# Kernel optimization log

Hardware: AMD Instinct MI355X
Metric: run time of the kernel (lower is better)

The kernel has to match this reference:

```python
import jax, jax.numpy as jnp
import numpy as np

B, N, D, H, DH, DEPTH = 4, 1024, 1024, 16, 64, 4
FI = int(D * 4.0 * 2 / 3)  # 2730, GEGLU inner dim
EPS = 1.1920929e-07  # torch float32 eps (RMSNorm default)
NEG = -jnp.finfo(jnp.float32).max


def rms(x, w):
    return x * jax.lax.rsqrt(jnp.mean(x * x, axis=-1, keepdims=True) + EPS) * w


def rope(t):
    # t: [b, h, n, d]; interleaved-pair rotary (lucidrains rotary_embedding_torch)
    n, d = t.shape[-2], t.shape[-1]
    inv_freq = 1.0 / (10000.0 ** (jnp.arange(0, d, 2, dtype=jnp.float32) / d))
    ang = jnp.arange(n, dtype=jnp.float32)[:, None] * inv_freq  # [n, d/2]
    cos = jnp.repeat(jnp.cos(ang), 2, axis=-1)  # [n, d]
    sin = jnp.repeat(jnp.sin(ang), 2, axis=-1)
    x = t.reshape(t.shape[:-1] + (d // 2, 2))
    rot = jnp.stack([-x[..., 1], x[..., 0]], axis=-1).reshape(t.shape)
    return t * cos + rot * sin


def setup_inputs() -> dict:
    key = jax.random.key(0)
    ks = jax.random.split(key, 14)
    s = 0.02
    return {
        "x": jax.random.normal(ks[0], (B, N, D), dtype=jnp.float32),
        "norm_attn_w": jnp.ones((DEPTH, D), jnp.float32),
        "wq": jax.random.normal(ks[1], (DEPTH, H * DH, D), jnp.float32) * s,
        "wkv": jax.random.normal(ks[2], (DEPTH, 2 * H * DH, D), jnp.float32) * s,
        "wo": jax.random.normal(ks[3], (DEPTH, D, H * DH), jnp.float32) * s,
        "wg": jax.random.normal(ks[4], (DEPTH, H, D), jnp.float32) * s,
        "wmix": jax.random.normal(ks[5], (DEPTH, H, D), jnp.float32) * s,
        "norm_ff_w": jnp.ones((DEPTH, D), jnp.float32),
        "ff_norm_w": jnp.ones((DEPTH, D), jnp.float32),
        "w_in": jax.random.normal(ks[6], (DEPTH, 2 * FI, D), jnp.float32) * s,
        "b_in": jnp.zeros((DEPTH, 2 * FI), jnp.float32),
        "w_out": jax.random.normal(ks[7], (DEPTH, D, FI), jnp.float32) * s,
        "b_out": jnp.zeros((DEPTH, D), jnp.float32),
        "final_norm_w": jnp.ones((D,), jnp.float32),
    }


def _forward(x, norm_attn_w, wq, wkv, wo, wg, wmix, norm_ff_w, ff_norm_w,
             w_in, b_in, w_out, b_out, final_norm_w):
    scale = DH ** -0.5
    causal = jnp.triu(jnp.ones((N, N), bool), k=1)  # True = masked
    value_residual = None
    for i in range(DEPTH):
        # --- attention block (pre-RMSNorm wrapper) ---
        h = rms(x, norm_attn_w[i])  # [b, n, d]
        q = jnp.einsum('bnd,ed->bne', h, wq[i]) * scale
        kv = jnp.einsum('bnd,ed->bne', h, wkv[i])
        k, v = jnp.split(kv, 2, axis=-1)
        split = lambda t: t.reshape(B, N, H, DH).transpose(0, 2, 1, 3)  # b h n d
        q, k, v = split(q), split(k), split(v)
        orig_v = v
        if value_residual is not None:
            mix = jax.nn.sigmoid(jnp.einsum('bnd,hd->bhn', h, wmix[i]))[..., None]
            v = v + mix * (value_residual - v)  # lerp(v, value_residual, mix)
        q, k = rope(q), rope(k)
        sim = jnp.einsum('bhid,bhjd->bhij', q, k)
        sim = jnp.where(causal, NEG, sim)
        attn = jax.nn.softmax(sim, axis=-1)
        out = jnp.einsum('bhij,bhjd->bhid', attn, v)
        gates = jax.nn.sigmoid(jnp.einsum('bnd,hd->bhn', h, wg[i]))[..., None]
        out = out * gates
        out = out.transpose(0, 2, 1, 3).reshape(B, N, H * DH)
        x = x + jnp.einsum('bne,de->bnd', out, wo[i])
        if value_residual is None:
            value_residual = orig_v
        # --- feedforward block (wrapper norm + FF's own pre-rmsnorm) ---
        g = rms(x, norm_ff_w[i])
        g = rms(g, ff_norm_w[i])
        u = jnp.einsum('bnd,ed->bne', g, w_in[i]) + b_in[i]
        a, gt = jnp.split(u, 2, axis=-1)
        u = a * jax.nn.gelu(gt, approximate=False)
        x = x + jnp.einsum('bnf,df->bnd', u, w_out[i]) + b_out[i]
    return rms(x, final_norm_w)


def reference(x, norm_attn_w, wq, wkv, wo, wg, wmix, norm_ff_w, ff_norm_w,
              w_in, b_in, w_out, b_out, final_norm_w):
    return _forward(x, norm_attn_w, wq, wkv, wo, wg, wmix, norm_ff_w,
                    ff_norm_w, w_in, b_in, w_out, b_out, final_norm_w)
```

## Files before the change

kernel.cpp:

```cpp
#include <hip/hip_runtime.h>
#include <cstdint>
#include <cstddef>


#define DEV_INLINE __device__ __forceinline__

typedef short bf16x8 __attribute__((ext_vector_type(8)));
typedef float f32x4 __attribute__((ext_vector_type(4)));

constexpr int Bsz = 4, Nseq = 1024, Dm = 1024, Hh = 16, DH = 64, NDEPTH = 4;
constexpr int FI = 2730;
constexpr int FI_PAD = 2752;
constexpr int FI_TILE = 2816;
constexpr int WIDE = 2 * FI_TILE;
constexpr int ROWS = Bsz * Nseq;
constexpr float EPSR = 1.1920929e-07f;

DEV_INLINE float bf2f(unsigned short u) {
  unsigned int x = ((unsigned int)u) << 16;
  float f; __builtin_memcpy(&f, &x, 4); return f;
}
DEV_INLINE unsigned short f2bf(float f) {
  unsigned int x; __builtin_memcpy(&x, &f, 4);
  unsigned int r = x + 0x7fffu + ((x >> 16) & 1u);
  return (unsigned short)(r >> 16);
}

using gptr_t = const __attribute__((address_space(1))) void*;
using lptr_t = __attribute__((address_space(3))) void*;
DEV_INLINE void gl_lds16(const void* g, void* l) {
  __builtin_amdgcn_global_load_lds((gptr_t)g, (lptr_t)l, 16, 0, 0);
}
DEV_INLINE void fence_mem() { asm volatile("" ::: "memory"); }

__global__ __launch_bounds__(256)
void convf2b(const float* __restrict__ src, unsigned short* __restrict__ dst,
             int src_rows, int src_cols, int dst_cols) {
  const int r = blockIdx.y;
  const int c8 = (blockIdx.x * blockDim.x + threadIdx.x) * 8;
  if (c8 >= dst_cols) return;
  alignas(16) unsigned short o[8];
  if (r < src_rows && c8 + 8 <= src_cols) {
    const float2* p = (const float2*)&src[(size_t)r * src_cols + c8];
    const float2 v0 = p[0], v1 = p[1], v2 = p[2], v3 = p[3];
    o[0] = f2bf(v0.x); o[1] = f2bf(v0.y); o[2] = f2bf(v1.x); o[3] = f2bf(v1.y);
    o[4] = f2bf(v2.x); o[5] = f2bf(v2.y); o[6] = f2bf(v3.x); o[7] = f2bf(v3.y);
  } else {
#pragma unroll
    for (int j = 0; j < 8; ++j) {
      const int c = c8 + j;
      float v = (r < src_rows && c < src_cols) ? src[(size_t)r * src_cols + c] : 0.0f;
      o[j] = f2bf(v);
    }
  }
  *(uint4*)&dst[(size_t)r * dst_cols + c8] = *(const uint4*)o;
}

__global__ __launch_bounds__(128)
void convf2b_g16(const float* __restrict__ src, unsigned short* __restrict__ dst) {
  const int p = blockIdx.y;
  const int c8 = threadIdx.x * 8;
  const int t = p >> 5, r5 = p & 31;
  const int half = (r5 < 16) ? 1 : 0;
  const int srow = t * 16 + (r5 & 15);
  alignas(16) unsigned short o[8];
  if (srow < FI) {
    const size_t base = ((size_t)((r5 < 16) ? 0 : 1) * FI + srow) * 1024 + c8;
    const float4 v0 = *(const float4*)&src[base];
    const float4 v1 = *(const float4*)&src[base + 4];
    o[0]=f2bf(v0.x); o[1]=f2bf(v0.y); o[2]=f2bf(v0.z); o[3]=f2bf(v0.w);
    o[4]=f2bf(v1.x); o[5]=f2bf(v1.y); o[6]=f2bf(v1.z); o[7]=f2bf(v1.w);
  } else {
#pragma unroll
    for (int j = 0; j < 8; ++j) o[j] = 0;
  }
  (void)half;
  *(uint4*)&dst[(size_t)p * 1024 + c8] = *(const uint4*)o;
}

__global__ __launch_bounds__(256)
void rope_tables(float* __restrict__ cost, float* __restrict__ sint) {
  int idx = blockIdx.x * 256 + threadIdx.x;
  if (idx >= Nseq * 32) return;
  int n = idx >> 5, p = idx & 31;
  float freq = powf(10000.0f, -(float)(2 * p) * (1.0f / 64.0f));
  float ang = (float)n * freq;
  cost[idx] = cosf(ang);
  sint[idx] = sinf(ang);
}

__global__ __launch_bounds__(256)
void rms_one(const float* __restrict__ x, const float* __restrict__ w,
             unsigned short* __restrict__ out) {
  __shared__ float sred[4];
  const int row = blockIdx.x, tid = threadIdx.x;
  const float4 v = ((const float4*)(x + (size_t)row * Dm))[tid];
  float ss = v.x * v.x + v.y * v.y + v.z * v.z + v.w * v.w;
#pragma unroll
  for (int o = 32; o >= 1; o >>= 1) ss += __shfl_xor(ss, o, 64);
  if ((tid & 63) == 0) sred[tid >> 6] = ss;
  __syncthreads();
  float rs = rsqrtf((sred[0] + sred[1] + sred[2] + sred[3]) * (1.0f / Dm) + EPSR);
  const float4 wv = ((const float4*)w)[tid];
  alignas(8) unsigned short o4[4] = { f2bf(v.x * rs * wv.x), f2bf(v.y * rs * wv.y),
                                      f2bf(v.z * rs * wv.z), f2bf(v.w * rs * wv.w) };
  *(uint2*)&out[(size_t)row * Dm + tid * 4] = *(const uint2*)o4;
}

__global__ __launch_bounds__(256)
void rms_ff(const float* __restrict__ x, const float* __restrict__ w1,
            const float* __restrict__ w2, unsigned short* __restrict__ out) {
  __shared__ float sred[4];
  const int row = blockIdx.x, tid = threadIdx.x;
  const float4 v = ((const float4*)(x + (size_t)row * Dm))[tid];
  const float4 w1v = ((const float4*)w1)[tid];
  const float4 w2v = ((const float4*)w2)[tid];
  float ss = v.x * v.x + v.y * v.y + v.z * v.z + v.w * v.w;
#pragma unroll
  for (int o = 32; o >= 1; o >>= 1) ss += __shfl_xor(ss, o, 64);
  if ((tid & 63) == 0) sred[tid >> 6] = ss;
  __syncthreads();
  float rs1 = rsqrtf((sred[0] + sred[1] + sred[2] + sred[3]) * (1.0f / Dm) + EPSR);
  float t0 = v.x * rs1 * w1v.x, t1 = v.y * rs1 * w1v.y;
  float t2 = v.z * rs1 * w1v.z, t3 = v.w * rs1 * w1v.w;
  float ss2 = t0 * t0 + t1 * t1 + t2 * t2 + t3 * t3;
#pragma unroll
  for (int o = 32; o >= 1; o >>= 1) ss2 += __shfl_xor(ss2, o, 64);
  __syncthreads();
  if ((tid & 63) == 0) sred[tid >> 6] = ss2;
  __syncthreads();
  float rs2 = rsqrtf((sred[0] + sred[1] + sred[2] + sred[3]) * (1.0f / Dm) + EPSR);
  alignas(8) unsigned short o4[4] = { f2bf(t0 * rs2 * w2v.x), f2bf(t1 * rs2 * w2v.y),
                                      f2bf(t2 * rs2 * w2v.z), f2bf(t3 * rs2 * w2v.w) };
  *(uint2*)&out[(size_t)row * Dm + tid * 4] = *(const uint2*)o4;
}

__global__ __launch_bounds__(256)
void rms_final(const float* __restrict__ x, const float* __restrict__ w,
               float* __restrict__ out) {
  __shared__ float sred[4];
  const int row = blockIdx.x, tid = threadIdx.x;
  const float4 v = ((const float4*)(x + (size_t)row * Dm))[tid];
  float ss = v.x * v.x + v.y * v.y + v.z * v.z + v.w * v.w;
#pragma unroll
  for (int o = 32; o >= 1; o >>= 1) ss += __shfl_xor(ss, o, 64);
  if ((tid & 63) == 0) sred[tid >> 6] = ss;
  __syncthreads();
  float rs = rsqrtf((sred[0] + sred[1] + sred[2] + sred[3]) * (1.0f / Dm) + EPSR);
  const float4 wv = ((const float4*)w)[tid];
  float4 o;
  o.x = v.x * rs * wv.x; o.y = v.y * rs * wv.y;
  o.z = v.z * rs * wv.z; o.w = v.w * rs * wv.w;
  ((float4*)(out + (size_t)row * Dm))[tid] = o;
}

template <int MODE>
__global__ __launch_bounds__(256)
void gemm_nt(const unsigned short* __restrict__ A,
             const unsigned short* __restrict__ Bw,
             void* __restrict__ Cout,
             const float* __restrict__ bias,
             const float* __restrict__ resid,
             int K, int ldc, int n_store) {
  __shared__ unsigned short As[2][128 * 64];
  __shared__ unsigned short Bs[2][128 * 64];
  const int tid = threadIdx.x;
  const int m0 = blockIdx.x * 128;
  const int n0 = blockIdx.y * 128;
  const int w = tid >> 6, l = tid & 63;
  const int wm = (w >> 1) * 64, wn = (w & 1) * 64;
  const int lr = l & 15, lg = l >> 4;
  const int lsub = l & 7, lrow8 = l >> 3;
  const int colsw = (lsub ^ lrow8) << 3;
  const unsigned short* gA = &A[(size_t)(m0 + w * 8 + lrow8) * K + colsw];
  const unsigned short* gB = &Bw[(size_t)(n0 + w * 8 + lrow8) * K + colsw];
  const size_t rstep = (size_t)32 * K;
  f32x4 acc[4][4] = {};

  auto stage = [&](int buf, int kt) {
    const int o = kt * 64;
#pragma unroll
    for (int i = 0; i < 4; ++i) {
      gl_lds16(gA + i * rstep + o, &As[buf][i * 2048 + w * 512]);
      gl_lds16(gB + i * rstep + o, &Bs[buf][i * 2048 + w * 512]);
    }
  };
  auto compute = [&](int buf) {
    bf16x8 af[2][4], bfr[2][4];
#pragma unroll
    for (int ks = 0; ks < 2; ++ks) {
      const int slot = (ks * 4 + lg) ^ (lr & 7);
#pragma unroll
      for (int fj = 0; fj < 4; ++fj)
        bfr[ks][fj] = *(const bf16x8*)&Bs[buf][(wn + fj * 16 + lr) * 64 + slot * 8];
#pragma unroll
      for (int fi = 0; fi < 4; ++fi)
        af[ks][fi] = *(const bf16x8*)&As[buf][(wm + fi * 16 + lr) * 64 + slot * 8];
    }
    __builtin_amdgcn_s_setprio(1);
#pragma unroll
    for (int ks = 0; ks < 2; ++ks)
#pragma unroll
      for (int fi = 0; fi < 4; ++fi)
#pragma unroll
        for (int fj = 0; fj < 4; ++fj)
          acc[fi][fj] = __builtin_amdgcn_mfma_f32_16x16x32_bf16(af[ks][fi], bfr[ks][fj], acc[fi][fj], 0, 0, 0);
    __builtin_amdgcn_s_setprio(0);
  };

  const int nk = K >> 6;
  stage(0, 0);
  asm volatile("s_waitcnt vmcnt(0)" ::: "memory");
  __builtin_amdgcn_s_barrier();
  fence_mem();
  int cur = 0;
#pragma unroll 1
  for (int kt = 0; kt < nk; ++kt) {
    const bool more = (kt + 1 < nk);
    if (more) stage(cur ^ 1, kt + 1);
    compute(cur);
    if (more) {
      asm volatile("s_waitcnt vmcnt(0)" ::: "memory");
      __builtin_amdgcn_s_barrier();
      fence_mem();
    }
    cur ^= 1;
  }

#pragma unroll
  for (int fi = 0; fi < 4; ++fi) {
    const int rowb = m0 + wm + fi * 16 + lg * 4;
#pragma unroll
    for (int fj = 0; fj < 4; ++fj) {
      const int col = n0 + wn + fj * 16 + lr;
#pragma unroll
      for (int r = 0; r < 4; ++r) {
        const float val = acc[fi][fj][r];
        const int rr = rowb + r;
        if constexpr (MODE == 1) {
          if (col < n_store)
            ((float*)Cout)[(size_t)rr * ldc + col] = 1.0f / (1.0f + __expf(-val));
        } else {
          const float bv = bias ? bias[col] : 0.0f;
          ((float*)Cout)[(size_t)rr * ldc + col] =
              resid[(size_t)rr * ldc + col] + val + bv;
        }
      }
    }
  }
}

template <int MODE>
__global__ __launch_bounds__(512)
void gemm_nt256(const unsigned short* __restrict__ A,
                const unsigned short* __restrict__ Bw,
                void* __restrict__ Cout,
                const float* __restrict__ bias,
                int K, int ldc) {
  __shared__ unsigned short As[2][256 * 64];
  __shared__ unsigned short Bs[2][256 * 64];
  const int tid = threadIdx.x;
  const int m0 = blockIdx.x * 256;
  const int n0 = blockIdx.y * 256;
  const int w = tid >> 6, l = tid & 63;
  const int wm = (w >> 2) * 128, wn = (w & 3) * 64;
  const int lr = l & 15, lg = l >> 4;
  const int lsub = l & 7, lrow8 = l >> 3;
  const int colsw = (lsub ^ lrow8) << 3;
  const unsigned short* gA = &A[(size_t)(m0 + w * 8 + lrow8) * K + colsw];
  const unsigned short* gB = &Bw[(size_t)(n0 + w * 8 + lrow8) * K + colsw];
  const size_t rstep = (size_t)64 * K;
  f32x4 acc[8][4] = {};

  auto stage = [&](int buf, int kt) {
    const int o = kt * 64;
#pragma unroll
    for (int i = 0; i < 4; ++i) {
      gl_lds16(gA + i * rstep + o, &As[buf][i * 4096 + w * 512]);
      gl_lds16(gB + i * rstep + o, &Bs[buf][i * 4096 + w * 512]);
    }
  };
  auto compute = [&](int buf) {
#pragma unroll
    for (int ks = 0; ks < 2; ++ks) {
      const int slot = (ks * 4 + lg) ^ (lr & 7);
      bf16x8 bfr[4], af[8];
#pragma unroll
      for (int fj = 0; fj < 4; ++fj)
        bfr[fj] = *(const bf16x8*)&Bs[buf][(wn + fj * 16 + lr) * 64 + slot * 8];
#pragma unroll
      for (int fi = 0; fi < 8; ++fi)
        af[fi] = *(const bf16x8*)&As[buf][(wm + fi * 16 + lr) * 64 + slot * 8];
      __builtin_amdgcn_s_setprio(1);
#pragma unroll
      for (int fi = 0; fi < 8; ++fi)
#pragma unroll
        for (int fj = 0; fj < 4; ++fj)
          acc[fi][fj] = __builtin_amdgcn_mfma_f32_16x16x32_bf16(af[fi], bfr[fj], acc[fi][fj], 0, 0, 0);
      __builtin_amdgcn_s_setprio(0);
    }
  };

  const int nk = K >> 6;
  stage(0, 0);
  asm volatile("s_waitcnt vmcnt(0)" ::: "memory");
  __builtin_amdgcn_s_barrier();
  fence_mem();
  int cur = 0;
#pragma unroll 1
  for (int kt = 0; kt < nk; ++kt) {
    const bool more = (kt + 1 < nk);
    if (more) stage(cur ^ 1, kt + 1);
    compute(cur);
    if (more) {
      asm volatile("s_waitcnt vmcnt(0)" ::: "memory");
      __builtin_amdgcn_s_barrier();
      fence_mem();
    }
    cur ^= 1;
  }

#pragma unroll
  for (int fi = 0; fi < 8; ++fi) {
    const int rowb = m0 + wm + fi * 16 + lg * 4;
    if constexpr (MODE == 0) {
#pragma unroll
      for (int fj = 0; fj < 4; ++fj) {
        const int col = n0 + wn + fj * 16 + lr;
#pragma unroll
        for (int r = 0; r < 4; ++r)
          ((unsigned short*)Cout)[(size_t)(rowb + r) * ldc + col] = f2bf(acc[fi][fj][r]);
      }
    } else {
#pragma unroll
      for (int fjp = 0; fjp < 2; ++fjp) {
        const int ucol = ((n0 + wn) >> 1) + fjp * 16 + lr;
        if (ucol >= FI_PAD) continue;
        const bool live = (ucol < FI);
        const float ba = live ? bias[ucol] : 0.0f;
        const float bg = live ? bias[FI + ucol] : 0.0f;
#pragma unroll
        for (int r = 0; r < 4; ++r) {
          const float va = acc[fi][2 * fjp][r] + ba;
          const float vg = acc[fi][2 * fjp + 1][r] + bg;
          const float gel = 0.5f * vg * (1.0f + erff(vg * 0.70710678118654752f));
          ((unsigned short*)Cout)[(size_t)(rowb + r) * ldc + ucol] =
              f2bf(live ? va * gel : 0.0f);
        }
      }
    }
  }
}

__global__ __launch_bounds__(256)
void rope_qk(const unsigned short* __restrict__ qkv_lin,
             const float* __restrict__ cost, const float* __restrict__ sint,
             unsigned short* __restrict__ qb, unsigned short* __restrict__ kb) {
  const int nt = blockIdx.x, bh = blockIdx.y;
  const int b = bh >> 4, h = bh & 15;
  const int tid = threadIdx.x;
  const int pi = tid & 31, r0 = tid >> 5;
  const float scale = 0.125f;
#pragma unroll
  for (int j = 0; j < 8; ++j) {
    const int n = nt * 64 + r0 + j * 8;
    const int nf = b * Nseq + n;
    const float c = cost[n * 32 + pi], s = sint[n * 32 + pi];
    const unsigned short* qp = &qkv_lin[(size_t)nf * 3072 + h * 64 + pi * 2];
    float q0 = bf2f(qp[0]), q1 = bf2f(qp[1]);
    alignas(4) unsigned short oq[2];
    oq[0] = f2bf((q0 * c - q1 * s) * scale);
    oq[1] = f2bf((q1 * c + q0 * s) * scale);
    *(unsigned int*)&qb[((size_t)bh * Nseq + n) * 64 + pi * 2] = *(const unsigned int*)oq;
    const unsigned short* kp = &qkv_lin[(size_t)nf * 3072 + 1024 + h * 64 + pi * 2];
    float k0 = bf2f(kp[0]), k1 = bf2f(kp[1]);
    alignas(4) unsigned short ok[2];
    ok[0] = f2bf(k0 * c - k1 * s);
    ok[1] = f2bf(k1 * c + k0 * s);
    *(unsigned int*)&kb[((size_t)bh * Nseq + n) * 64 + pi * 2] = *(const unsigned int*)ok;
  }
}

__global__ __launch_bounds__(256)
void v_mix_pack(const unsigned short* __restrict__ qkv_lin,
                const float* __restrict__ gm,
                unsigned short* __restrict__ vres,
                unsigned short* __restrict__ vtb, int layer) {
  __shared__ unsigned short T[64][72];
  const int nt = blockIdx.x, bh = blockIdx.y;
  const int b = bh >> 4, h = bh & 15;
  const int tid = threadIdx.x;
#pragma unroll
  for (int p = 0; p < 2; ++p) {
    int c = tid + p * 256;
    int nl = c >> 3, cg = (c & 7) << 3;
    int n = nt * 64 + nl, nf = b * Nseq + n;
    uint4 vv = *(const uint4*)&qkv_lin[(size_t)nf * 3072 + 2048 + h * 64 + cg];
    if (layer == 0) {
      *(uint4*)&vres[((size_t)bh * Nseq + n) * 64 + cg] = vv;
      *(uint4*)&T[nl][cg] = vv;
    } else {
      alignas(16) unsigned short ve[8]; *(uint4*)ve = vv;
      uint4 rv = *(const uint4*)&vres[((size_t)bh * Nseq + n) * 64 + cg];
      alignas(16) unsigned short re[8]; *(uint4*)re = rv;
      const float mix = gm[(size_t)nf * 32 + 16 + h];
      alignas(16) unsigned short oe[8];
#pragma unroll
      for (int j = 0; j < 8; ++j) {
        float v = bf2f(ve[j]), rr = bf2f(re[j]);
        oe[j] = f2bf(v + mix * (rr - v));
      }
      *(uint4*)&T[nl][cg] = *(const uint4*)oe;
    }
  }
  __syncthreads();
#pragma unroll
  for (int p = 0; p < 2; ++p) {
    int c = tid + p * 256;
    int d = c >> 3, ng = (c & 7) << 3;
    alignas(16) unsigned short oe[8];
#pragma unroll
    for (int j = 0; j < 8; ++j) oe[j] = T[ng + j][d];
    *(uint4*)&vtb[(size_t)bh * 65536 + (size_t)d * Nseq + nt * 64 + ng] = *(const uint4*)oe;
  }
}

__global__ __launch_bounds__(256)
void attn_fwd(const unsigned short* __restrict__ qb,
              const unsigned short* __restrict__ kb,
              const unsigned short* __restrict__ vtb,
              const float* __restrict__ gm,
              unsigned short* __restrict__ attn_out) {
  __shared__ unsigned short Ps[4][16][72];
  const int bid = blockIdx.x;
  const int x = bid & 7, rest = bid >> 3;
  const int bh = x * 8 + (rest & 7);
  const int qt = 15 - (rest >> 3);
  const int b = bh >> 4, h = bh & 15;
  const int tid = threadIdx.x;
  const int w = tid >> 6, l = tid & 63;
  const int lr = l & 15, lg = l >> 4;
  const int q0 = qt * 64 + w * 16;
  const size_t head = (size_t)bh * Nseq * DH;

  bf16x8 aq[2];
  aq[0] = *(const bf16x8*)&qb[head + (size_t)(q0 + lr) * DH + lg * 8];
  aq[1] = *(const bf16x8*)&qb[head + (size_t)(q0 + lr) * DH + 32 + lg * 8];

  float mrow[4] = {-1e30f, -1e30f, -1e30f, -1e30f};
  float lsum[4] = {0.f, 0.f, 0.f, 0.f};
  f32x4 acco[4] = {};

  for (int kt = 0; kt <= qt; ++kt) {
    const int kv0 = kt * 64;
    f32x4 s[4];
#pragma unroll
    for (int t = 0; t < 4; ++t) {
      bf16x8 bk0 = *(const bf16x8*)&kb[head + (size_t)(kv0 + t * 16 + lr) * DH + lg * 8];
      bf16x8 bk1 = *(const bf16x8*)&kb[head + (size_t)(kv0 + t * 16 + lr) * DH + 32 + lg * 8];
      f32x4 z = {};
      z = __builtin_amdgcn_mfma_f32_16x16x32_bf16(aq[0], bk0, z, 0, 0, 0);
      z = __builtin_amdgcn_mfma_f32_16x16x32_bf16(aq[1], bk1, z, 0, 0, 0);
      s[t] = z;
    }
    const bool diag = (kt == qt);
    float mx4[4];
    bool need = false;
#pragma unroll
    for (int r = 0; r < 4; ++r) {
      const int qr = q0 + lg * 4 + r;
      float mx = -1e30f;
#pragma unroll
      for (int t = 0; t < 4; ++t) {
        float sv = s[t][r];
        if (diag && (kv0 + t * 16 + lr > qr)) sv = -1e30f;
        s[t][r] = sv;
        mx = fmaxf(mx, sv);
      }
      mx = fmaxf(mx, __shfl_xor(mx, 1, 64));
      mx = fmaxf(mx, __shfl_xor(mx, 2, 64));
      mx = fmaxf(mx, __shfl_xor(mx, 4, 64));
      mx = fmaxf(mx, __shfl_xor(mx, 8, 64));
      mx4[r] = mx;
      need = need || (mx > mrow[r] + 8.0f);
    }
    if (__any(need)) {
#pragma unroll
      for (int r = 0; r < 4; ++r) {
        const float mn = fmaxf(mrow[r], mx4[r]);
        const float alpha = __expf(mrow[r] - mn);
        mrow[r] = mn;
        lsum[r] *= alpha;
#pragma unroll
        for (int dt = 0; dt < 4; ++dt) acco[dt][r] *= alpha;
      }
    }
#pragma unroll
    for (int r = 0; r < 4; ++r) {
      float rs = 0.f;
#pragma unroll
      for (int t = 0; t < 4; ++t) {
        float pv = __expf(s[t][r] - mrow[r]);
        s[t][r] = pv;
        rs += pv;
      }
      rs += __shfl_xor(rs, 1, 64);
      rs += __shfl_xor(rs, 2, 64);
      rs += __shfl_xor(rs, 4, 64);
      rs += __shfl_xor(rs, 8, 64);
      lsum[r] += rs;
    }
#pragma unroll
    for (int t = 0; t < 4; ++t)
#pragma unroll
      for (int r = 0; r < 4; ++r)
        Ps[w][lg * 4 + r][t * 16 + lr] = f2bf(s[t][r]);
#pragma unroll
    for (int ks = 0; ks < 2; ++ks) {
      bf16x8 ap = *(const bf16x8*)&Ps[w][lr][ks * 32 + lg * 8];
#pragma unroll
      for (int dt = 0; dt < 4; ++dt) {
        bf16x8 bv = *(const bf16x8*)&vtb[head + (size_t)(dt * 16 + lr) * Nseq + kv0 + ks * 32 + lg * 8];
        acco[dt] = __builtin_amdgcn_mfma_f32_16x16x32_bf16(ap, bv, acco[dt], 0, 0, 0);
      }
    }
  }
#pragma unroll
  for (int r = 0; r < 4; ++r) {
    const int qr = q0 + lg * 4 + r;
    const int nf = b * Nseq + qr;
    const float gate = gm[(size_t)nf * 32 + h];
    const float inv = 1.0f / lsum[r];
#pragma unroll
    for (int dt = 0; dt < 4; ++dt)
      attn_out[(size_t)nf * Dm + h * DH + dt * 16 + lr] = f2bf(acco[dt][r] * inv * gate);
  }
}

extern "C" void kernel_launch(void* const* d_in, const int* in_sizes, int n_in,
                              void* d_out, int out_size, void* d_ws, size_t ws_size,
                              hipStream_t stream) {
  const float* x_in  = (const float*)d_in[0];
  const float* naw   = (const float*)d_in[1];
  const float* wq    = (const float*)d_in[2];
  const float* wkv   = (const float*)d_in[3];
  const float* wo    = (const float*)d_in[4];
  const float* wg    = (const float*)d_in[5];
  const float* wmix  = (const float*)d_in[6];
  const float* nfw   = (const float*)d_in[7];
  const float* ffw   = (const float*)d_in[8];
  const float* w_in  = (const float*)d_in[9];
  const float* b_in  = (const float*)d_in[10];
  const float* w_out = (const float*)d_in[11];
  const float* b_out = (const float*)d_in[12];
  const float* fnw   = (const float*)d_in[13];

  uint8_t* ws = (uint8_t*)d_ws;
  size_t off = 0;
  auto alloc = [&](size_t bytes) -> void* {
    void* p = ws + off;
    off += (bytes + 255) & ~(size_t)255;
    return p;
  };
  float*          x_res    = (float*)alloc((size_t)ROWS * Dm * 4);
  unsigned short* h        = (unsigned short*)alloc((size_t)ROWS * Dm * 2);
  unsigned short* qkv_lin  = (unsigned short*)alloc((size_t)ROWS * 3072 * 2);
  float*          gm       = (float*)alloc((size_t)ROWS * 32 * 4);
  unsigned short* qb       = (unsigned short*)alloc((size_t)64 * Nseq * DH * 2);
  unsigned short* kb       = (unsigned short*)alloc((size_t)64 * Nseq * DH * 2);
  unsigned short* vtb      = (unsigned short*)alloc((size_t)64 * Nseq * DH * 2);
  unsigned short* vres     = (unsigned short*)alloc((size_t)64 * Nseq * DH * 2);
  unsigned short* attn     = (unsigned short*)alloc((size_t)ROWS * Dm * 2);
  float*          cost     = (float*)alloc((size_t)Nseq * 32 * 4);
  float*          sint     = (float*)alloc((size_t)Nseq * 32 * 4);
  unsigned short* wqkv_bf  = (unsigned short*)alloc((size_t)3072 * 1024 * 2);
  unsigned short* wo_bf    = (unsigned short*)alloc((size_t)1024 * 1024 * 2);
  unsigned short* wgm_bf   = (unsigned short*)alloc((size_t)128 * 1024 * 2);
  unsigned short* win_bf   = (unsigned short*)alloc((size_t)WIDE * 1024 * 2);
  unsigned short* wout_bf  = (unsigned short*)alloc((size_t)1024 * FI_PAD * 2);
  unsigned short* u = qkv_lin;

  hipMemcpyAsync(x_res, x_in, (size_t)ROWS * Dm * 4, hipMemcpyDeviceToDevice, stream);
  rope_tables<<<128, 256, 0, stream>>>(cost, sint);

  for (int i = 0; i < NDEPTH; ++i) {
    convf2b<<<dim3(1, 1024), 128, 0, stream>>>(wq + (size_t)i * 1024 * 1024, wqkv_bf, 1024, 1024, 1024);
    convf2b<<<dim3(1, 2048), 128, 0, stream>>>(wkv + (size_t)i * 2048 * 1024, wqkv_bf + (size_t)1024 * 1024, 2048, 1024, 1024);
    convf2b<<<dim3(1, 1024), 128, 0, stream>>>(wo + (size_t)i * 1024 * 1024, wo_bf, 1024, 1024, 1024);
    convf2b<<<dim3(1, 16), 128, 0, stream>>>(wg + (size_t)i * 16 * 1024, wgm_bf, 16, 1024, 1024);
    convf2b<<<dim3(1, 16), 128, 0, stream>>>(wmix + (size_t)i * 16 * 1024, wgm_bf + 16 * 1024, 16, 1024, 1024);
    convf2b<<<dim3(1, 96), 128, 0, stream>>>(wg, wgm_bf + 32 * 1024, 0, 1024, 1024);
    convf2b_g16<<<dim3(1, WIDE), 128, 0, stream>>>(w_in + (size_t)i * 2 * FI * 1024, win_bf);
    convf2b<<<dim3(2, 1024), 256, 0, stream>>>(w_out + (size_t)i * 1024 * FI, wout_bf, 1024, FI, FI_PAD);

    rms_one<<<ROWS, 256, 0, stream>>>(x_res, naw + i * 1024, h);
    gemm_nt256<0><<<dim3(16, 12), 512, 0, stream>>>(h, wqkv_bf, qkv_lin, nullptr, 1024, 3072);
    gemm_nt<1><<<dim3(32, 1), 256, 0, stream>>>(h, wgm_bf, gm, nullptr, nullptr, 1024, 32, 32);
    rope_qk<<<dim3(16, 64), 256, 0, stream>>>(qkv_lin, cost, sint, qb, kb);
    v_mix_pack<<<dim3(16, 64), 256, 0, stream>>>(qkv_lin, gm, vres, vtb, i);
    attn_fwd<<<1024, 256, 0, stream>>>(qb, kb, vtb, gm, attn);
    gemm_nt<2><<<dim3(32, 8), 256, 0, stream>>>(attn, wo_bf, x_res, nullptr, x_res, 1024, 1024, 1024);
    rms_ff<<<ROWS, 256, 0, stream>>>(x_res, nfw + i * 1024, ffw + i * 1024, h);
    gemm_nt256<3><<<dim3(16, 22), 512, 0, stream>>>(h, win_bf, u, b_in + (size_t)i * 2 * FI, 1024, FI_PAD);
    gemm_nt<2><<<dim3(32, 8), 256, 0, stream>>>(u, wout_bf, x_res, b_out + i * 1024, x_res, FI_PAD, 1024, 1024);
  }
  rms_final<<<ROWS, 256, 0, stream>>>(x_res, fnw, (float*)d_out);
}
```

Baseline: 1.553 ms.

## Interleave staged loads with MFMA quarters and remap workgroups across XCDs in 256-tile GEMM

The 256x256 GEMM kernel now splits each k-step into four quarters. Each quarter issues one part of the next tile's global-to-LDS loads, and barriers are inserted between quarters so memory traffic is spread across the compute. Workgroups are launched as a 1D grid and remapped so consecutive tiles land on the same XCD, aiming for better L2 reuse. Launch bounds now request 2 waves per EU. The extra barriers may add synchronisation cost, and the occupancy hint may pressure registers given the 32 accumulators.

```diff
diff --git a/kernel.cpp b/kernel.cpp
--- a/kernel.cpp
+++ b/kernel.cpp
@@ -61,7 +61,6 @@
   const int p = blockIdx.y;
   const int c8 = threadIdx.x * 8;
   const int t = p >> 5, r5 = p & 31;
-  const int half = (r5 < 16) ? 1 : 0;
   const int srow = t * 16 + (r5 & 15);
   alignas(16) unsigned short o[8];
   if (srow < FI) {
@@ -74,7 +73,6 @@
 #pragma unroll
     for (int j = 0; j < 8; ++j) o[j] = 0;
   }
-  (void)half;
   *(uint4*)&dst[(size_t)p * 1024 + c8] = *(const uint4*)o;
 }
 
@@ -251,17 +249,21 @@
 }
 
 template <int MODE>
-__global__ __launch_bounds__(512)
+__global__ __launch_bounds__(512, 2)
 void gemm_nt256(const unsigned short* __restrict__ A,
                 const unsigned short* __restrict__ Bw,
                 void* __restrict__ Cout,
                 const float* __restrict__ bias,
-                int K, int ldc) {
+                int K, int ldc, int nm, int nn) {
   __shared__ unsigned short As[2][256 * 64];
   __shared__ unsigned short Bs[2][256 * 64];
   const int tid = threadIdx.x;
-  const int m0 = blockIdx.x * 256;
-  const int n0 = blockIdx.y * 256;
+  const int nwg = nm * nn;
+  const int qq = nwg >> 3;
+  const int xcd = blockIdx.x & 7, orig = blockIdx.x >> 3;
+  const int wgid = xcd * qq + orig;
+  const int m0 = (wgid % nm) * 256;
+  const int n0 = (wgid / nm) * 256;
   const int w = tid >> 6, l = tid & 63;
   const int wm = (w >> 2) * 128, wn = (w & 3) * 64;
   const int lr = l & 15, lg = l >> 4;
@@ -272,52 +274,62 @@
   const size_t rstep = (size_t)64 * K;
   f32x4 acc[8][4] = {};
 
-  auto stage = [&](int buf, int kt) {
+  auto stage_part = [&](int buf, int kt, int part) {
     const int o = kt * 64;
-#pragma unroll
-    for (int i = 0; i < 4; ++i) {
-      gl_lds16(gA + i * rstep + o, &As[buf][i * 4096 + w * 512]);
-      gl_lds16(gB + i * rstep + o, &Bs[buf][i * 4096 + w * 512]);
+    const int i0 = (part & 1) * 2;
+    if (part < 2) {
+      gl_lds16(gA + (size_t)i0 * rstep + o,       &As[buf][i0 * 4096 + w * 512]);
+      gl_lds16(gA + (size_t)(i0 + 1) * rstep + o, &As[buf][(i0 + 1) * 4096 + w * 512]);
+    } else {
+      gl_lds16(gB + (size_t)i0 * rstep + o,       &Bs[buf][i0 * 4096 + w * 512]);
+      gl_lds16(gB + (size_t)(i0 + 1) * rstep + o, &Bs[buf][(i0 + 1) * 4096 + w * 512]);
     }
   };
-  auto compute = [&](int buf) {
-#pragma unroll
-    for (int ks = 0; ks < 2; ++ks) {
-      const int slot = (ks * 4 + lg) ^ (lr & 7);
-      bf16x8 bfr[4], af[8];
-#pragma unroll
-      for (int fj = 0; fj < 4; ++fj)
-        bfr[fj] = *(const bf16x8*)&Bs[buf][(wn + fj * 16 + lr) * 64 + slot * 8];
-#pragma unroll
-      for (int fi = 0; fi < 8; ++fi)
-        af[fi] = *(const bf16x8*)&As[buf][(wm + fi * 16 + lr) * 64 + slot * 8];
-      __builtin_amdgcn_s_setprio(1);
-#pragma unroll
-      for (int fi = 0; fi < 8; ++fi)
-#pragma unroll
-        for (int fj = 0; fj < 4; ++fj)
-          acc[fi][fj] = __builtin_amdgcn_mfma_f32_16x16x32_bf16(af[fi], bfr[fj], acc[fi][fj], 0, 0, 0);
-      __builtin_amdgcn_s_setprio(0);
-    }
-  };
 
   const int nk = K >> 6;
-  stage(0, 0);
+  stage_part(0, 0, 0); stage_part(0, 0, 1);
+  stage_part(0, 0, 2); stage_part(0, 0, 3);
   asm volatile("s_waitcnt vmcnt(0)" ::: "memory");
   __builtin_amdgcn_s_barrier();
   fence_mem();
-  int cur = 0;
+
 #pragma unroll 1
-  for (int kt = 0; kt < nk; ++kt) {
-    const bool more = (kt + 1 < nk);
-    if (more) stage(cur ^ 1, kt + 1);
-    compute(cur);
+  for (int t = 0; t < nk; ++t) {
+    const int p = t & 1;
+    const bool more = (t + 1 < nk);
+    bf16x8 bfr[4];
+#pragma unroll
+    for (int q = 0; q < 4; ++q) {
+      const int ks = q >> 1, half = q & 1;
+      const int slot = (ks * 4 + lg) ^ (lr & 7);
+      if (half == 0) {
+#pragma unroll
+        for (int fj = 0; fj < 4; ++fj)
+          bfr[fj] = *(const bf16x8*)&Bs[p][(wn + fj * 16 + lr) * 64 + slot * 8];
+      }
+      bf16x8 af[4];
+#pragma unroll
+      for (int fi = 0; fi < 4; ++fi)
+        af[fi] = *(const bf16x8*)&As[p][(wm + half * 64 + fi * 16 + lr) * 64 + slot * 8];
+      if (more) stage_part(p ^ 1, t + 1, q);
+      __builtin_amdgcn_s_setprio(1);
+#pragma unroll
+      for (int fi = 0; fi < 4; ++fi)
+#pragma unroll
+        for (int fj = 0; fj < 4; ++fj)
+          acc[half * 4 + fi][fj] =
+              __builtin_amdgcn_mfma_f32_16x16x32_bf16(af[fi], bfr[fj], acc[half * 4 + fi][fj], 0, 0, 0);
+      __builtin_amdgcn_s_setprio(0);
+      if (q < 3) {
+        __builtin_amdgcn_s_barrier();
+        fence_mem();
+      }
+    }
     if (more) {
       asm volatile("s_waitcnt vmcnt(0)" ::: "memory");
       __builtin_amdgcn_s_barrier();
       fence_mem();
     }
-    cur ^= 1;
   }
 
 #pragma unroll
@@ -594,14 +606,14 @@
     convf2b<<<dim3(2, 1024), 256, 0, stream>>>(w_out + (size_t)i * 1024 * FI, wout_bf, 1024, FI, FI_PAD);
 
     rms_one<<<ROWS, 256, 0, stream>>>(x_res, naw + i * 1024, h);
-    gemm_nt256<0><<<dim3(16, 12), 512, 0, stream>>>(h, wqkv_bf, qkv_lin, nullptr, 1024, 3072);
+    gemm_nt256<0><<<192, 512, 0, stream>>>(h, wqkv_bf, qkv_lin, nullptr, 1024, 3072, 16, 12);
     gemm_nt<1><<<dim3(32, 1), 256, 0, stream>>>(h, wgm_bf, gm, nullptr, nullptr, 1024, 32, 32);
     rope_qk<<<dim3(16, 64), 256, 0, stream>>>(qkv_lin, cost, sint, qb, kb);
     v_mix_pack<<<dim3(16, 64), 256, 0, stream>>>(qkv_lin, gm, vres, vtb, i);
     attn_fwd<<<1024, 256, 0, stream>>>(qb, kb, vtb, gm, attn);
     gemm_nt<2><<<dim3(32, 8), 256, 0, stream>>>(attn, wo_bf, x_res, nullptr, x_res, 1024, 1024, 1024);
     rms_ff<<<ROWS, 256, 0, stream>>>(x_res, nfw + i * 1024, ffw + i * 1024, h);
-    gemm_nt256<3><<<dim3(16, 22), 512, 0, stream>>>(h, win_bf, u, b_in + (size_t)i * 2 * FI, 1024, FI_PAD);
+    gemm_nt256<3><<<352, 512, 0, stream>>>(h, win_bf, u, b_in + (size_t)i * 2 * FI, 1024, FI_PAD, 16, 22);
     gemm_nt<2><<<dim3(32, 8), 256, 0, stream>>>(u, wout_bf, x_res, b_out + i * 1024, x_res, FI_PAD, 1024, 1024);
   }
   rms_final<<<ROWS, 256, 0, stream>>>(x_res, fnw, (float*)d_out);
```

After: 1.520 ms. 2.2% less time.
